# Kernel optimization log

Hardware: AMD Instinct MI355X
Metric: run time of the kernel (lower is better)

## Reference

```python
import jax, jax.numpy as jnp
import numpy as np
import math

EMBED_DIMS = 256
NUM_HEADS = 8
NUM_LEVELS = 4
NUM_POINTS = 8
SPATIAL_SHAPES = np.array([[92, 160], [46, 80], [23, 40], [12, 20]], dtype=np.int32)


def _offset_bias():
    # Faithful to reset_parameters(): per-head unit directions scaled by point index.
    thetas = np.arange(NUM_HEADS, dtype=np.float32) * (2.0 * math.pi / NUM_HEADS)
    grid = np.stack([np.cos(thetas), np.sin(thetas)], axis=-1)
    grid = grid / np.abs(grid).max(axis=-1, keepdims=True)
    grid = np.tile(grid[:, None, None, :], (1, NUM_LEVELS, NUM_POINTS, 1))
    for i in range(NUM_POINTS):
        grid[:, :, i, :] *= i + 1
    return grid.reshape(-1).astype(np.float32)


def setup_inputs() -> dict:
    key = jax.random.key(0)
    ks = jax.random.split(key, 8)
    B, Q, E = 4, 10000, EMBED_DIMS
    S = int((SPATIAL_SHAPES[:, 0] * SPATIAL_SHAPES[:, 1]).sum())
    Z = 4  # num_z_anchors; NUM_POINTS % Z == 0
    query = jax.random.normal(ks[0], (B, Q, E), dtype=jnp.float32)
    value = jax.random.normal(ks[1], (B, S, E), dtype=jnp.float32)
    reference_points = jax.random.uniform(ks[2], (B, Q, Z, 2), dtype=jnp.float32)
    # Learned params (random weights so the math is fully exercised; bias per original init).
    w_off = jax.random.normal(ks[3], (E, NUM_HEADS * NUM_LEVELS * NUM_POINTS * 2), dtype=jnp.float32) * 0.01
    b_off = jnp.asarray(_offset_bias())
    w_attn = jax.random.normal(ks[4], (E, NUM_HEADS * NUM_LEVELS * NUM_POINTS), dtype=jnp.float32) * 0.02
    b_attn = jnp.zeros((NUM_HEADS * NUM_LEVELS * NUM_POINTS,), dtype=jnp.float32)
    w_val = jax.random.normal(ks[5], (E, E), dtype=jnp.float32) * (1.0 / np.sqrt(E))
    b_val = jnp.zeros((E,), dtype=jnp.float32)
    return {
        "query": query, "value": value, "reference_points": reference_points,
        "w_off": w_off, "b_off": b_off, "w_attn": w_attn, "b_attn": b_attn,
        "w_val": w_val, "b_val": b_val,
        "spatial_shapes": jnp.asarray(SPATIAL_SHAPES),
    }


def _bilinear_sample(img, px, py):
    """grid_sample(bilinear, padding=zeros, align_corners=False).
    img: [N, H, W, D]; px, py: [N, Q, P] in pixel coords. Returns [N, Q, P, D]."""
    H, W = img.shape[1], img.shape[2]
    x0 = jnp.floor(px); y0 = jnp.floor(py)
    wx = (px - x0)[..., None]; wy = (py - y0)[..., None]
    x0i = x0.astype(jnp.int32); y0i = y0.astype(jnp.int32)
    x1i = x0i + 1; y1i = y0i + 1
    bidx = jnp.arange(img.shape[0])[:, None, None]
    def gather(yy, xx):
        m = ((yy >= 0) & (yy < H) & (xx >= 0) & (xx < W)).astype(img.dtype)[..., None]
        return img[bidx, jnp.clip(yy, 0, H - 1), jnp.clip(xx, 0, W - 1)] * m
    v00 = gather(y0i, x0i); v01 = gather(y0i, x1i)
    v10 = gather(y1i, x0i); v11 = gather(y1i, x1i)
    return (v00 * (1 - wx) + v01 * wx) * (1 - wy) + (v10 * (1 - wx) + v11 * wx) * wy


def _forward(query, value, reference_points, w_off, b_off, w_attn, b_attn, w_val, b_val, shapes_np):
    B, Q, E = query.shape
    NH, L, NP = NUM_HEADS, shapes_np.shape[0], NUM_POINTS
    D = E // NH
    v = (value @ w_val + b_val).reshape(B, -1, NH, D)  # [B, S, NH, D]
    off = (query @ w_off + b_off).reshape(B, Q, NH, L, NP, 2)
    attn = jax.nn.softmax((query @ w_attn + b_attn).reshape(B, Q, NH, L * NP), axis=-1)
    attn = attn.reshape(B, Q, NH, L, NP)
    # Normalize offsets by (W, H) per level.
    norm = jnp.asarray(np.stack([shapes_np[:, 1], shapes_np[:, 0]], axis=-1), dtype=off.dtype)  # [L,2]
    off = off / norm[None, None, None, :, None, :]
    Z = reference_points.shape[2]
    off = off.reshape(B, Q, NH, L, NP // Z, Z, 2)
    loc = reference_points[:, :, None, None, None, :, :] + off  # [B,Q,NH,L,NP/Z,Z,2]
    loc = loc.reshape(B, Q, NH, L, NP, 2)
    out = jnp.zeros((B, Q, NH, D), dtype=query.dtype)
    start = 0
    for lvl in range(L):
        hl, wl = int(shapes_np[lvl, 0]), int(shapes_np[lvl, 1])
        seg = v[:, start:start + hl * wl]
        start += hl * wl
        img = seg.reshape(B, hl, wl, NH, D).transpose(0, 3, 1, 2, 4).reshape(B * NH, hl, wl, D)
        g = loc[:, :, :, lvl].transpose(0, 2, 1, 3, 4).reshape(B * NH, Q, NP, 2)
        # align_corners=False: pixel = norm_coord * size - 0.5
        px = g[..., 0] * wl - 0.5
        py = g[..., 1] * hl - 0.5
        samp = _bilinear_sample(img, px, py)  # [B*NH, Q, NP, D]
        w = attn[:, :, :, lvl].transpose(0, 2, 1, 3).reshape(B * NH, Q, NP)
        out = out + jnp.einsum('nqpd,nqp->nqd', samp, w).reshape(B, NH, Q, D).transpose(0, 2, 1, 3)
    return out.reshape(B, Q, NH * D)


def reference(query, value, reference_points, w_off, b_off, w_attn, b_attn, w_val, b_val, spatial_shapes):
    shapes_np = np.asarray(spatial_shapes)
    return _forward(query, value, reference_points, w_off, b_off, w_attn, b_attn, w_val, b_val, shapes_np)
```

## Files before the change

kernel.cpp:

```cpp
#include <hip/hip_runtime.h>

#define BATCH    4
#define NQ       10000
#define EMB      256
#define NH       8
#define DH       32
#define NL       4
#define NP       8
#define S_TOTAL  19560
#define NROW     (BATCH * NQ)
#define VROWS    (BATCH * S_TOTAL)

typedef _Float16 half8 __attribute__((ext_vector_type(8)));
typedef _Float16 half4v __attribute__((ext_vector_type(4)));
typedef _Float16 half2v __attribute__((ext_vector_type(2)));
typedef float floatx4 __attribute__((ext_vector_type(4)));

__global__ __launch_bounds__(256) void transp_swz(
    const float* __restrict__ W, _Float16* __restrict__ WTs, int N) {
  const int tid = blockIdx.x * 256 + threadIdx.x;
  const int n = tid >> 8, k = tid & 255;
  const int c = k >> 3, e = k & 7;
  WTs[(size_t)n * 256 + (((c ^ (n & 7)) << 3) + e)] = (_Float16)W[(size_t)k * N + n];
}

__global__ __launch_bounds__(256) void bias_cat(
    const float* __restrict__ b0, const float* __restrict__ b1,
    float* __restrict__ o) {
  const int t = blockIdx.x * 256 + threadIdx.x;
  if (t < 512) o[t] = b0[t];
  else if (t < 768) o[t] = b1[t - 512];
}

template <int NC, int NYS, bool SWZ>
__global__ __launch_bounds__(256, 2) void gemm4(
    const float* __restrict__ A, const _Float16* __restrict__ WTs,
    const float* __restrict__ bias, _Float16* __restrict__ C, int M) {
  __shared__ _Float16 bsm[64 * 256];
  const int t = threadIdx.x;
  const int wave = t >> 6, lane = t & 63;
  const int l15 = lane & 15, quad = lane >> 4;
  const int m0 = blockIdx.x * 256 + wave * 64;
  const int nlo = blockIdx.y * (NC / NYS);
  const int nchunks = (NC / NYS) / 64;

  half8 a[4][8];
  #pragma unroll
  for (int i = 0; i < 4; ++i) {
    const float* Ar = A + (size_t)min(m0 + 16 * i + l15, M - 1) * 256 + quad * 8;
    #pragma unroll
    for (int ks = 0; ks < 8; ++ks) {
      const float4 f0 = *(const float4*)(Ar + ks * 32);
      const float4 f1 = *(const float4*)(Ar + ks * 32 + 4);
      a[i][ks][0] = (_Float16)f0.x; a[i][ks][1] = (_Float16)f0.y;
      a[i][ks][2] = (_Float16)f0.z; a[i][ks][3] = (_Float16)f0.w;
      a[i][ks][4] = (_Float16)f1.x; a[i][ks][5] = (_Float16)f1.y;
      a[i][ks][6] = (_Float16)f1.z; a[i][ks][7] = (_Float16)f1.w;
    }
  }

  const _Float16* src = WTs + (size_t)nlo * 256;

  for (int ch = 0; ch < nchunks; ++ch) {
    __syncthreads();
    #pragma unroll
    for (int i = 0; i < 8; ++i)
      *(half8*)&bsm[t * 8 + i * 2048] = *(const half8*)(src + t * 8 + i * 2048);
    __syncthreads();

    floatx4 acc[4][4] = {};
    #pragma unroll
    for (int ks = 0; ks < 8; ++ks) {
      half8 b[4];
      #pragma unroll
      for (int j = 0; j < 4; ++j)
        b[j] = *(const half8*)&bsm[(16 * j + l15) * 256 +
                                   ((((ks * 4 + quad) ^ (l15 & 7))) << 3)];
      #pragma unroll
      for (int j = 0; j < 4; ++j)
        #pragma unroll
        for (int i = 0; i < 4; ++i)
          acc[i][j] = __builtin_amdgcn_mfma_f32_16x16x32_f16(a[i][ks], b[j], acc[i][j], 0, 0, 0);
    }

    const int nc0 = nlo + ch * 64;
    float bc[4];
    #pragma unroll
    for (int j = 0; j < 4; ++j) bc[j] = bias[nc0 + 16 * j + l15];

    #pragma unroll
    for (int i = 0; i < 4; ++i) {
      #pragma unroll
      for (int r = 0; r < 4; ++r) {
        const int row = m0 + 16 * i + quad * 4 + r;
        if (row < M) {
          if (SWZ) {
            const int b = row / S_TOTAL;
            const int s = row - b * S_TOTAL;
            #pragma unroll
            for (int j = 0; j < 4; ++j) {
              const int col = nc0 + 16 * j + l15;
              const size_t dst =
                  (((size_t)b * NH + (col >> 5)) * S_TOTAL + s) * 32 + (col & 31);
              C[dst] = (_Float16)(acc[i][j][r] + bc[j]);
            }
          } else {
            #pragma unroll
            for (int j = 0; j < 4; ++j)
              C[(size_t)row * NC + nc0 + 16 * j + l15] =
                  (_Float16)(acc[i][j][r] + bc[j]);
          }
        }
      }
    }
    src += 64 * 256;
  }
}

__global__ __launch_bounds__(256) void msda_sample(
    const _Float16* __restrict__ vproj,
    const _Float16* __restrict__ fused,
    const float* __restrict__ ref,
    float* __restrict__ out) {
  const int lvl_h[NL] = {92, 46, 23, 12};
  const int lvl_w[NL] = {160, 80, 40, 20};
  const int lvl_s[NL] = {0, 14720, 18400, 19320};

  __shared__ int   addr_s[512];
  __shared__ float wl_s[512];
  __shared__ float wr_s[512];

  const int t   = threadIdx.x;
  const int blk = blockIdx.x;
  const int b   = blk & 3;
  const int q   = blk >> 2;
  const int row = b * NQ + q;

  const int h  = t >> 5;
  const int lp = t & 31;
  const int l  = lp >> 3;
  const int p  = lp & 7;

  const float logit = (float)fused[(size_t)row * 768 + 512 + t];
  float mxv = logit;
  #pragma unroll
  for (int m = 1; m < 32; m <<= 1) mxv = fmaxf(mxv, __shfl_xor(mxv, m));
  const float e = __expf(logit - mxv);
  float sum = e;
  #pragma unroll
  for (int m = 1; m < 32; m <<= 1) sum += __shfl_xor(sum, m);
  const float attnw = e / sum;

  const half2v o2 = *(const half2v*)(fused + (size_t)row * 768 + 2 * t);
  const float ox = (float)o2[0], oy = (float)o2[1];
  const int z = p & 3;
  const float rx = ref[((size_t)row * 4 + z) * 2 + 0];
  const float ry = ref[((size_t)row * 4 + z) * 2 + 1];
  const int Wl = lvl_w[l], Hl = lvl_h[l], st = lvl_s[l];

  const float px = fmaf(rx, (float)Wl, ox) - 0.5f;
  const float py = fmaf(ry, (float)Hl, oy) - 0.5f;
  const float x0f = floorf(px), y0f = floorf(py);
  const float wx = px - x0f, wy = py - y0f;
  const int x0 = (int)x0f, y0 = (int)y0f;
  const int x1 = x0 + 1,   y1 = y0 + 1;

  const float mx0 = (x0 >= 0 && x0 < Wl) ? 1.f : 0.f;
  const float mx1 = (x1 >= 0 && x1 < Wl) ? 1.f : 0.f;
  const float my0 = (y0 >= 0 && y0 < Hl) ? 1.f : 0.f;
  const float my1 = (y1 >= 0 && y1 < Hl) ? 1.f : 0.f;
  const int xb  = min(max(x0, -1), Wl - 1);
  const int cy0 = min(max(y0, 0), Hl - 1);
  const int cy1 = min(max(y1, 0), Hl - 1);

  const int bh   = b * NH + h;
  const int lbase = bh * S_TOTAL + st;
  const float wlc = attnw * (1.f - wx) * mx0;
  const float wrc = attnw * wx * mx1;

  addr_s[2 * t + 0] = (lbase + cy0 * Wl + xb) * 32;
  addr_s[2 * t + 1] = (lbase + cy1 * Wl + xb) * 32;
  wl_s[2 * t + 0] = wlc * (1.f - wy) * my0;
  wr_s[2 * t + 0] = wrc * (1.f - wy) * my0;
  wl_s[2 * t + 1] = wlc * wy * my1;
  wr_s[2 * t + 1] = wrc * wy * my1;
  __syncthreads();

  const int g  = t & 31;
  const int c  = g & 7;
  const int sd = (g >> 3) & 1;
  const int ph = g >> 4;
  const int ldoff = sd * 32 + 4 * c;

  float a0 = 0.f, a1 = 0.f, a2 = 0.f, a3 = 0.f;
  #pragma unroll 8
  for (int i = 0; i < 16; ++i) {
    const int idx = ((h << 5) + 2 * i + ph) * 2;
    const int at = addr_s[idx],     ab = addr_s[idx + 1];
    const float wt = sd ? wr_s[idx]     : wl_s[idx];
    const float wb = sd ? wr_s[idx + 1] : wl_s[idx + 1];
    const half4v vt = *(const half4v*)(vproj + at + ldoff);
    const half4v vb = *(const half4v*)(vproj + ab + ldoff);
    a0 = fmaf(wt, (float)vt[0], a0); a1 = fmaf(wt, (float)vt[1], a1);
    a2 = fmaf(wt, (float)vt[2], a2); a3 = fmaf(wt, (float)vt[3], a3);
    a0 = fmaf(wb, (float)vb[0], a0); a1 = fmaf(wb, (float)vb[1], a1);
    a2 = fmaf(wb, (float)vb[2], a2); a3 = fmaf(wb, (float)vb[3], a3);
  }

  a0 += __shfl_xor(a0, 8);  a1 += __shfl_xor(a1, 8);
  a2 += __shfl_xor(a2, 8);  a3 += __shfl_xor(a3, 8);
  a0 += __shfl_xor(a0, 16); a1 += __shfl_xor(a1, 16);
  a2 += __shfl_xor(a2, 16); a3 += __shfl_xor(a3, 16);

  if (g < 8) {
    float4 o; o.x = a0; o.y = a1; o.z = a2; o.w = a3;
    *(float4*)(out + (size_t)row * 256 + (h << 5) + 4 * c) = o;
  }
}

extern "C" void kernel_launch(void* const* d_in, const int* in_sizes, int n_in,
                              void* d_out, int out_size, void* d_ws, size_t ws_size,
                              hipStream_t stream) {
  const float* query  = (const float*)d_in[0];
  const float* value  = (const float*)d_in[1];
  const float* refpts = (const float*)d_in[2];
  const float* w_off  = (const float*)d_in[3];
  const float* b_off  = (const float*)d_in[4];
  const float* w_attn = (const float*)d_in[5];
  const float* b_attn = (const float*)d_in[6];
  const float* w_val  = (const float*)d_in[7];
  const float* b_val  = (const float*)d_in[8];
  float* out = (float*)d_out;

  char* p = (char*)d_ws;
  p += 256;
  _Float16* vh    = (_Float16*)p;  p += (size_t)VROWS * 256 * 2;
  p += 256;
  _Float16* wT768 = (_Float16*)p;  p += (size_t)768 * 256 * 2;
  _Float16* wvaT  = (_Float16*)p;  p += (size_t)256 * 256 * 2;
  float*    bias768 = (float*)p;   p += 768 * 4;
  _Float16* fused_h = (_Float16*)p; p += (size_t)NROW * 768 * 2;

  transp_swz<<<512, 256, 0, stream>>>(w_off, wT768, 512);
  transp_swz<<<256, 256, 0, stream>>>(w_attn, wT768 + 512 * 256, 256);
  transp_swz<<<256, 256, 0, stream>>>(w_val, wvaT, 256);
  bias_cat<<<3, 256, 0, stream>>>(b_off, b_attn, bias768);

  gemm4<256, 1, true><<<dim3((VROWS + 255) / 256, 1), 256, 0, stream>>>(
      value, wvaT, b_val, vh, VROWS);
  gemm4<768, 2, false><<<dim3((NROW + 255) / 256, 2), 256, 0, stream>>>(
      query, wT768, bias768, fused_h, NROW);

  msda_sample<<<dim3(NROW), 256, 0, stream>>>(vh, fused_h, refpts, out);
}
```

Before: 482.1 us.

## Merge weight-prep launches, shrink GEMM row tiles, batch sampler gathers

Replaces the three transpose kernels and the bias concat with a single prep kernel, and has the GEMM read the two bias arrays directly. The GEMM row tile drops from 256 to 128 rows per block (32 per wave) with launch bounds raised to 3 blocks per CU, which gives more blocks and higher occupancy but reloads the B tile from LDS for fewer rows each time. The sampler now issues all 32 gathers into registers before any FMA, to expose memory-level parallelism, and asks for 4 blocks per CU. The cost is higher register pressure in the sampler and less weight reuse in the GEMM.

```diff
diff --git a/kernel.cpp b/kernel.cpp
--- a/kernel.cpp
+++ b/kernel.cpp
@@ -16,37 +16,38 @@
 typedef _Float16 half2v __attribute__((ext_vector_type(2)));
 typedef float floatx4 __attribute__((ext_vector_type(4)));
 
-__global__ __launch_bounds__(256) void transp_swz(
-    const float* __restrict__ W, _Float16* __restrict__ WTs, int N) {
+__global__ __launch_bounds__(256) void prep_weights(
+    const float* __restrict__ w_off, const float* __restrict__ w_attn,
+    const float* __restrict__ w_val, _Float16* __restrict__ wT768,
+    _Float16* __restrict__ wvaT) {
   const int tid = blockIdx.x * 256 + threadIdx.x;
   const int n = tid >> 8, k = tid & 255;
   const int c = k >> 3, e = k & 7;
-  WTs[(size_t)n * 256 + (((c ^ (n & 7)) << 3) + e)] = (_Float16)W[(size_t)k * N + n];
-}
-
-__global__ __launch_bounds__(256) void bias_cat(
-    const float* __restrict__ b0, const float* __restrict__ b1,
-    float* __restrict__ o) {
-  const int t = blockIdx.x * 256 + threadIdx.x;
-  if (t < 512) o[t] = b0[t];
-  else if (t < 768) o[t] = b1[t - 512];
+  const int swz = ((c ^ (n & 7)) << 3) + e;
+  float v;
+  _Float16* dst;
+  if (n < 512)      { v = w_off[(size_t)k * 512 + n];          dst = wT768 + (size_t)n * 256; }
+  else if (n < 768) { v = w_attn[(size_t)k * 256 + (n - 512)]; dst = wT768 + (size_t)n * 256; }
+  else              { v = w_val[(size_t)k * 256 + (n - 768)];  dst = wvaT + (size_t)(n - 768) * 256; }
+  dst[swz] = (_Float16)v;
 }
 
 template <int NC, int NYS, bool SWZ>
-__global__ __launch_bounds__(256, 2) void gemm4(
+__global__ __launch_bounds__(256, 3) void gemm5(
     const float* __restrict__ A, const _Float16* __restrict__ WTs,
-    const float* __restrict__ bias, _Float16* __restrict__ C, int M) {
+    const float* __restrict__ bias0, const float* __restrict__ bias1,
+    int splitc, _Float16* __restrict__ C, int M) {
   __shared__ _Float16 bsm[64 * 256];
   const int t = threadIdx.x;
   const int wave = t >> 6, lane = t & 63;
   const int l15 = lane & 15, quad = lane >> 4;
-  const int m0 = blockIdx.x * 256 + wave * 64;
+  const int m0 = blockIdx.x * 128 + wave * 32;
   const int nlo = blockIdx.y * (NC / NYS);
   const int nchunks = (NC / NYS) / 64;
 
-  half8 a[4][8];
-  #pragma unroll
-  for (int i = 0; i < 4; ++i) {
+  half8 a[2][8];
+  #pragma unroll
+  for (int i = 0; i < 2; ++i) {
     const float* Ar = A + (size_t)min(m0 + 16 * i + l15, M - 1) * 256 + quad * 8;
     #pragma unroll
     for (int ks = 0; ks < 8; ++ks) {
@@ -68,7 +69,7 @@
       *(half8*)&bsm[t * 8 + i * 2048] = *(const half8*)(src + t * 8 + i * 2048);
     __syncthreads();
 
-    floatx4 acc[4][4] = {};
+    floatx4 acc[2][4] = {};
     #pragma unroll
     for (int ks = 0; ks < 8; ++ks) {
       half8 b[4];
@@ -79,17 +80,20 @@
       #pragma unroll
       for (int j = 0; j < 4; ++j)
         #pragma unroll
-        for (int i = 0; i < 4; ++i)
+        for (int i = 0; i < 2; ++i)
           acc[i][j] = __builtin_amdgcn_mfma_f32_16x16x32_f16(a[i][ks], b[j], acc[i][j], 0, 0, 0);
     }
 
     const int nc0 = nlo + ch * 64;
     float bc[4];
     #pragma unroll
-    for (int j = 0; j < 4; ++j) bc[j] = bias[nc0 + 16 * j + l15];
-
-    #pragma unroll
-    for (int i = 0; i < 4; ++i) {
+    for (int j = 0; j < 4; ++j) {
+      const int col = nc0 + 16 * j + l15;
+      bc[j] = (col < splitc) ? bias0[col] : bias1[col - splitc];
+    }
+
+    #pragma unroll
+    for (int i = 0; i < 2; ++i) {
       #pragma unroll
       for (int r = 0; r < 4; ++r) {
         const int row = m0 + 16 * i + quad * 4 + r;
@@ -117,7 +121,7 @@
   }
 }
 
-__global__ __launch_bounds__(256) void msda_sample(
+__global__ __launch_bounds__(256, 4) void msda_sample(
     const _Float16* __restrict__ vproj,
     const _Float16* __restrict__ fused,
     const float* __restrict__ ref,
@@ -192,19 +196,25 @@
   const int ph = g >> 4;
   const int ldoff = sd * 32 + 4 * c;
 
-  float a0 = 0.f, a1 = 0.f, a2 = 0.f, a3 = 0.f;
-  #pragma unroll 8
+  half4v vt[16], vb[16];
+  float wt[16], wb[16];
+  #pragma unroll
   for (int i = 0; i < 16; ++i) {
     const int idx = ((h << 5) + 2 * i + ph) * 2;
-    const int at = addr_s[idx],     ab = addr_s[idx + 1];
-    const float wt = sd ? wr_s[idx]     : wl_s[idx];
-    const float wb = sd ? wr_s[idx + 1] : wl_s[idx + 1];
-    const half4v vt = *(const half4v*)(vproj + at + ldoff);
-    const half4v vb = *(const half4v*)(vproj + ab + ldoff);
-    a0 = fmaf(wt, (float)vt[0], a0); a1 = fmaf(wt, (float)vt[1], a1);
-    a2 = fmaf(wt, (float)vt[2], a2); a3 = fmaf(wt, (float)vt[3], a3);
-    a0 = fmaf(wb, (float)vb[0], a0); a1 = fmaf(wb, (float)vb[1], a1);
-    a2 = fmaf(wb, (float)vb[2], a2); a3 = fmaf(wb, (float)vb[3], a3);
+    const int at = addr_s[idx], ab = addr_s[idx + 1];
+    wt[i] = sd ? wr_s[idx]     : wl_s[idx];
+    wb[i] = sd ? wr_s[idx + 1] : wl_s[idx + 1];
+    vt[i] = *(const half4v*)(vproj + at + ldoff);
+    vb[i] = *(const half4v*)(vproj + ab + ldoff);
+  }
+
+  float a0 = 0.f, a1 = 0.f, a2 = 0.f, a3 = 0.f;
+  #pragma unroll
+  for (int i = 0; i < 16; ++i) {
+    a0 = fmaf(wt[i], (float)vt[i][0], a0); a1 = fmaf(wt[i], (float)vt[i][1], a1);
+    a2 = fmaf(wt[i], (float)vt[i][2], a2); a3 = fmaf(wt[i], (float)vt[i][3], a3);
+    a0 = fmaf(wb[i], (float)vb[i][0], a0); a1 = fmaf(wb[i], (float)vb[i][1], a1);
+    a2 = fmaf(wb[i], (float)vb[i][2], a2); a3 = fmaf(wb[i], (float)vb[i][3], a3);
   }
 
   a0 += __shfl_xor(a0, 8);  a1 += __shfl_xor(a1, 8);
@@ -238,18 +248,14 @@
   p += 256;
   _Float16* wT768 = (_Float16*)p;  p += (size_t)768 * 256 * 2;
   _Float16* wvaT  = (_Float16*)p;  p += (size_t)256 * 256 * 2;
-  float*    bias768 = (float*)p;   p += 768 * 4;
   _Float16* fused_h = (_Float16*)p; p += (size_t)NROW * 768 * 2;
 
-  transp_swz<<<512, 256, 0, stream>>>(w_off, wT768, 512);
-  transp_swz<<<256, 256, 0, stream>>>(w_attn, wT768 + 512 * 256, 256);
-  transp_swz<<<256, 256, 0, stream>>>(w_val, wvaT, 256);
-  bias_cat<<<3, 256, 0, stream>>>(b_off, b_attn, bias768);
-
-  gemm4<256, 1, true><<<dim3((VROWS + 255) / 256, 1), 256, 0, stream>>>(
-      value, wvaT, b_val, vh, VROWS);
-  gemm4<768, 2, false><<<dim3((NROW + 255) / 256, 2), 256, 0, stream>>>(
-      query, wT768, bias768, fused_h, NROW);
+  prep_weights<<<1024, 256, 0, stream>>>(w_off, w_attn, w_val, wT768, wvaT);
+
+  gemm5<256, 1, true><<<dim3((VROWS + 127) / 128, 1), 256, 0, stream>>>(
+      value, wvaT, b_val, b_val, 1 << 30, vh, VROWS);
+  gemm5<768, 2, false><<<dim3((NROW + 127) / 128, 2), 256, 0, stream>>>(
+      query, wT768, b_off, b_attn, 512, fused_h, NROW);
 
   msda_sample<<<dim3(NROW), 256, 0, stream>>>(vh, fused_h, refpts, out);
 }
```

Measured after the change: 402.8 us. -16.5%, faster.
